# Kernel optimization log

Hardware: AMD Instinct MI355X
Metric: run time of the kernel (lower is better)

The kernel has to match this reference:

```python
import jax, jax.numpy as jnp
import numpy as np

B, K, D, H, NIRREPS = 1024, 16, 1024, 16, 16  # batch, seq_len(=group n), input_dim, heads, n_irreps
HD = D // H


def setup_inputs() -> dict:
    key = jax.random.key(0)
    ks = jax.random.split(key, 10)
    s = 1.0 / np.sqrt(D)
    return {
        "x": jax.random.normal(ks[0], (B, K, D), jnp.float32),
        "projectors": jax.random.normal(ks[1], (NIRREPS, K, K), jnp.float32) * 0.25,
        "Wq": jax.random.normal(ks[2], (D, D), jnp.float32) * s,
        "bq": jnp.zeros((D,), jnp.float32),
        "Wk": jax.random.normal(ks[3], (D, D), jnp.float32) * s,
        "bk": jnp.zeros((D,), jnp.float32),
        "Wv": jax.random.normal(ks[4], (D, D), jnp.float32) * s,
        "bv": jnp.zeros((D,), jnp.float32),
        "Wo": jax.random.normal(ks[5], (D, D), jnp.float32) * s,
        "bo": jnp.zeros((D,), jnp.float32),
    }


def reference(x, projectors, Wq, bq, Wk, bk, Wv, bv, Wo, bo):
    b, k, d = x.shape
    hd = d // H
    # QKV projections -> [b, H, k, hd]
    def heads(t):
        return t.reshape(b, k, H, hd).transpose(0, 2, 1, 3)
    Q = heads(x @ Wq + bq)
    Kt = heads(x @ Wk + bk)
    V = heads(x @ Wv + bv)
    scale = jnp.asarray(1.0 / np.sqrt(hd), x.dtype)

    # Per-irrep: project Q/K/V along the seq axis with P, run masked-free softmax
    # attention on tiny k x k scores, accumulate over irreps (eval mode, no dropout).
    def body(acc, P):
        Qp = jnp.einsum('ij,bhjd->bhid', P, Q)
        Kp = jnp.einsum('ij,bhjd->bhid', P, Kt)
        Vp = jnp.einsum('ij,bhjd->bhid', P, V)
        scores = jnp.einsum('bhid,bhjd->bhij', Qp, Kp) * scale
        w = jax.nn.softmax(scores, axis=-1)
        return acc + jnp.einsum('bhij,bhjd->bhid', w, Vp), None

    total, _ = jax.lax.scan(body, jnp.zeros_like(V), projectors)
    # merge heads -> [b, k, d], then output projection
    out = total.transpose(0, 2, 1, 3).reshape(b, k, d) @ Wo + bo
    return out
```

## Files before the change

kernel.cpp:

```cpp
#include <hip/hip_runtime.h>


typedef unsigned short u16;
typedef unsigned int u32;
typedef __attribute__((ext_vector_type(8))) __bf16 bf16x8;
typedef __attribute__((ext_vector_type(4))) float f32x4;
typedef __attribute__((ext_vector_type(4))) u32 u32x4;
typedef __attribute__((ext_vector_type(4))) u16 u16x4;
typedef __attribute__((ext_vector_type(4))) float float4v;
typedef __attribute__((address_space(1))) void gvoid;
typedef __attribute__((address_space(3))) void svoid;

#define MFMA16(a, b, c) __builtin_amdgcn_mfma_f32_16x16x32_bf16(a, b, c, 0, 0, 0)

__device__ __forceinline__ u16 f2bf(float f) {
  u32 u = __builtin_bit_cast(u32, f);
  return (u16)((u + 0x7fffu + ((u >> 16) & 1u)) >> 16);
}
__device__ __forceinline__ float bf2f(u16 h) {
  u32 u = ((u32)h) << 16;
  return __builtin_bit_cast(float, u);
}
__device__ __forceinline__ float ld_bias(const void* p, int i, int isf32) {
  return isf32 ? ((const float*)p)[i] : bf2f(((const u16*)p)[i]);
}
__device__ __forceinline__ bf16x8 ld_frag(const u16* p) {
  u32x4 v = *reinterpret_cast<const u32x4*>(p);
  return __builtin_bit_cast(bf16x8, v);
}
__device__ __forceinline__ bf16x8 ld_frag_lo(const u16* p, int lane) {
  u32x4 v = {0u, 0u, 0u, 0u};
  if (lane < 32) v = *reinterpret_cast<const u32x4*>(p);
  return __builtin_bit_cast(bf16x8, v);
}
__device__ __forceinline__ void async16(const u16* g, u16* l) {
  __builtin_amdgcn_global_load_lds((gvoid*)g, (svoid*)l, 16, 0, 0);
}

__device__ __forceinline__ bf16x8 c2frag(f32x4 v, int lane) {
  const u32 p01 = ((u32)f2bf(v[1]) << 16) | (u32)f2bf(v[0]);
  const u32 p23 = ((u32)f2bf(v[3]) << 16) | (u32)f2bf(v[2]);
  const int base = (lane & 15) + ((lane & 16) << 1);
  u32x4 o;
  o[0] = (u32)__shfl((int)p01, base);
  o[1] = (u32)__shfl((int)p23, base);
  o[2] = (u32)__shfl((int)p01, base + 16);
  o[3] = (u32)__shfl((int)p23, base + 16);
  if (lane >= 32) o = (u32x4){0u, 0u, 0u, 0u};
  return __builtin_bit_cast(bf16x8, o);
}

__global__ __launch_bounds__(1024) void detect_dtype(const u32* __restrict__ x,
                                                     int* __restrict__ flag) {
  const int tid = threadIdx.x;
  int cnt = 0;
#pragma unroll
  for (int q = 0; q < 4; ++q) {
    const u32x4 v = ((const u32x4*)x)[q * 1024 + tid];
#pragma unroll
    for (int j = 0; j < 4; ++j) {
      const u32 e = (v[j] >> 23) & 0xffu;
      cnt += (e >= 64u && e <= 191u) ? 1 : 0;
    }
  }
  __shared__ int sred[16];
  for (int o = 32; o; o >>= 1) cnt += __shfl_down(cnt, o);
  if ((tid & 63) == 0) sred[tid >> 6] = cnt;
  __syncthreads();
  if (tid == 0) {
    int t = 0;
#pragma unroll
    for (int i = 0; i < 16; ++i) t += sred[i];
    flag[0] = (t > 8192) ? 1 : 0;
  }
}

__global__ __launch_bounds__(256) void convert_x(const void* __restrict__ src,
                                                 u16* __restrict__ dst,
                                                 const int* __restrict__ flag) {
  const int i4 = blockIdx.x * 256 + threadIdx.x;
  if (*flag) {
    const float4v v = ((const float4v*)src)[i4];
    u16x4 o;
#pragma unroll
    for (int j = 0; j < 4; ++j) o[j] = f2bf(v[j]);
    ((u16x4*)dst)[i4] = o;
  } else {
    ((u16x4*)dst)[i4] = ((const u16x4*)src)[i4];
  }
}

__global__ __launch_bounds__(256) void transpose_conv(
    const void* __restrict__ w0, const void* __restrict__ w1,
    const void* __restrict__ w2, const void* __restrict__ w3,
    u16* __restrict__ d0, u16* __restrict__ d1, u16* __restrict__ d2,
    u16* __restrict__ d3, const int* __restrict__ flag) {
  __shared__ u16 tile[32][33];
  const int z = blockIdx.z;
  const void* src = (z == 0) ? w0 : (z == 1) ? w1 : (z == 2) ? w2 : w3;
  u16* dst = (z == 0) ? d0 : (z == 1) ? d1 : (z == 2) ? d2 : d3;
  const int isf32 = *flag;
  const int tx = threadIdx.x & 31;
  const int ty = (threadIdx.x >> 5) * 4;
  const int bx = blockIdx.x * 32;
  const int by = blockIdx.y * 32;
#pragma unroll
  for (int r = 0; r < 4; ++r) {
    const int idx = (by + ty + r) * 1024 + bx + tx;
    tile[ty + r][tx] = isf32 ? f2bf(((const float*)src)[idx]) : ((const u16*)src)[idx];
  }
  __syncthreads();
#pragma unroll
  for (int r = 0; r < 4; ++r)
    dst[(bx + ty + r) * 1024 + by + tx] = tile[tx][ty + r];
}

template <int MODE>
__global__ __launch_bounds__(512, 2) void gemm256(
    const u16* __restrict__ X, const u16* __restrict__ Wt,
    const void* __restrict__ b0, const void* __restrict__ b1,
    const void* __restrict__ b2, void* __restrict__ o0, u16* __restrict__ o1,
    u16* __restrict__ o2, const int* __restrict__ flag) {
  __shared__ alignas(16) u16 sm[65536];
  const int tid = threadIdx.x;
  const int wave = tid >> 6, lane = tid & 63;
  const int fr = lane & 15, fq = lane >> 4;
  const int wm = wave >> 2, wn = wave & 3;
  const int isf32 = *flag;

  const int nwg = gridDim.x;
  const int per = nwg >> 3;
  const int bid = blockIdx.x;
  const int wg = (bid & 7) * per + (bid >> 3);
  const int m0 = (wg & 63) << 8;
  const int n0 = (wg >> 6) << 8;

  const int gl = ((tid & 7) ^ ((tid >> 3) & 7)) * 8;
  const u16* aS = X + (size_t)(m0 + (tid >> 3)) * 1024 + gl;
  const u16* bS = Wt + (size_t)(n0 + (tid >> 3)) * 1024 + gl;
  u16* dA = sm + wave * 512;
  u16* dB = sm + 16384 + wave * 512;

  const u16* aR = sm + (wm * 128 + fr) * 64;
  const u16* bR = sm + 16384 + (wn * 64 + fr) * 64;
  const int g0 = (fq ^ (fr & 7)) * 8;
  const int g1 = ((fq ^ (fr & 7)) ^ 4) * 8;

  f32x4 acc[2][4][4] = {};
  bf16x8 af[2][4][2], bf[4][2];

#define STG_A(BUF, H, KT)                                                     \
  do {                                                                        \
    async16(aS + (H * 128) * 1024 + (KT), dA + (BUF)*32768 + (H)*8192);       \
    async16(aS + (H * 128 + 64) * 1024 + (KT),                                \
            dA + (BUF)*32768 + (H)*8192 + 4096);                              \
  } while (0)
#define STG_B(BUF, H, KT)                                                     \
  do {                                                                        \
    async16(bS + (H * 128) * 1024 + (KT), dB + (BUF)*32768 + (H)*8192);       \
    async16(bS + (H * 128 + 64) * 1024 + (KT),                                \
            dB + (BUF)*32768 + (H)*8192 + 4096);                              \
  } while (0)
#define LDA_ALL(CH, KH, BUF)                                                  \
  do {                                                                        \
    af[CH][0][KH] = ld_frag(aR + (BUF)*32768 + (CH)*4096 + ((KH) ? g1 : g0)); \
    af[CH][1][KH] =                                                           \
        ld_frag(aR + (BUF)*32768 + (CH)*4096 + 1024 + ((KH) ? g1 : g0));      \
    af[CH][2][KH] =                                                           \
        ld_frag(aR + (BUF)*32768 + (CH)*4096 + 2048 + ((KH) ? g1 : g0));      \
    af[CH][3][KH] =                                                           \
        ld_frag(aR + (BUF)*32768 + (CH)*4096 + 3072 + ((KH) ? g1 : g0));      \
  } while (0)
#define LDB_ALL(KH, BUF)                                                      \
  do {                                                                        \
    bf[0][KH] = ld_frag(bR + (BUF)*32768 + ((KH) ? g1 : g0));                 \
    bf[1][KH] = ld_frag(bR + (BUF)*32768 + 1024 + ((KH) ? g1 : g0));          \
    bf[2][KH] = ld_frag(bR + (BUF)*32768 + 2048 + ((KH) ? g1 : g0));          \
    bf[3][KH] = ld_frag(bR + (BUF)*32768 + 3072 + ((KH) ? g1 : g0));          \
  } while (0)
#define MM1(CH, FI, KH)                                                       \
  acc[CH][FI][0] = MFMA16(af[CH][FI][KH], bf[0][KH], acc[CH][FI][0]);         \
  acc[CH][FI][1] = MFMA16(af[CH][FI][KH], bf[1][KH], acc[CH][FI][1]);         \
  acc[CH][FI][2] = MFMA16(af[CH][FI][KH], bf[2][KH], acc[CH][FI][2]);         \
  acc[CH][FI][3] = MFMA16(af[CH][FI][KH], bf[3][KH], acc[CH][FI][3]);
#define MM(CH, KH)                                                            \
  do {                                                                        \
    __builtin_amdgcn_s_setprio(1);                                            \
    MM1(CH, 0, KH) MM1(CH, 1, KH) MM1(CH, 2, KH) MM1(CH, 3, KH)               \
    __builtin_amdgcn_s_setprio(0);                                            \
  } while (0)
#define BARR                                                                  \
  __builtin_amdgcn_s_barrier();                                               \
  __builtin_amdgcn_sched_barrier(0)
#define WAITV(N) asm volatile("s_waitcnt vmcnt(" #N ")" ::: "memory")
#define WAITL asm volatile("s_waitcnt lgkmcnt(0)" ::: "memory")
#define SCHED __builtin_amdgcn_sched_barrier(0)

  STG_A(0, 0, 0);
  STG_A(0, 1, 0);
  STG_B(0, 0, 0);
  STG_B(0, 1, 0);
  STG_A(1, 0, 64);
  STG_A(1, 1, 64);
  WAITV(4);
  BARR;

  for (int it = 0; it < 7; ++it) {
    const int kof = it * 128;
    LDA_ALL(0, 0, 0);
    LDB_ALL(0, 0);
    LDA_ALL(1, 0, 0);
    STG_B(1, 0, kof + 64);
    BARR;
    MM(0, 0);
    BARR;
    LDA_ALL(0, 1, 0);
    LDA_ALL(1, 1, 0);
    STG_B(1, 1, kof + 64);
    BARR;
    MM(1, 0);
    WAITL;
    SCHED;
    BARR;
    LDB_ALL(1, 0);
    STG_A(0, 0, kof + 128);
    BARR;
    MM(0, 1);
    BARR;
    STG_A(0, 1, kof + 128);
    BARR;
    MM(1, 1);
    WAITV(4);
    SCHED;
    BARR;
    LDA_ALL(0, 0, 1);
    LDB_ALL(0, 1);
    LDA_ALL(1, 0, 1);
    STG_B(0, 0, kof + 128);
    BARR;
    MM(0, 0);
    BARR;
    LDA_ALL(0, 1, 1);
    LDA_ALL(1, 1, 1);
    STG_B(0, 1, kof + 128);
    BARR;
    MM(1, 0);
    WAITL;
    SCHED;
    BARR;
    LDB_ALL(1, 1);
    STG_A(1, 0, kof + 192);
    BARR;
    MM(0, 1);
    BARR;
    STG_A(1, 1, kof + 192);
    BARR;
    MM(1, 1);
    WAITV(4);
    SCHED;
    BARR;
  }

  {
    LDA_ALL(0, 0, 0);
    LDB_ALL(0, 0);
    LDA_ALL(1, 0, 0);
    LDA_ALL(0, 1, 0);
    LDA_ALL(1, 1, 0);
    LDB_ALL(1, 0);
    STG_B(1, 0, 960);
    STG_B(1, 1, 960);
    MM(0, 0);
    MM(1, 0);
    MM(0, 1);
    MM(1, 1);
    WAITV(0);
    BARR;
    LDA_ALL(0, 0, 1);
    LDB_ALL(0, 1);
    LDA_ALL(1, 0, 1);
    LDA_ALL(0, 1, 1);
    LDA_ALL(1, 1, 1);
    LDB_ALL(1, 1);
    MM(0, 0);
    MM(1, 0);
    MM(0, 1);
    MM(1, 1);
  }

  if constexpr (MODE == 0) {
    const int q = n0 >> 10;
    const int nb = (n0 & 1023) + wn * 64;
    const void* bp = (q == 0) ? b0 : ((q == 1) ? b1 : b2);
    u16* q0 = (u16*)o0;
#pragma unroll
    for (int ch = 0; ch < 2; ++ch)
#pragma unroll
      for (int fi = 0; fi < 4; ++fi) {
        const int mbase = m0 + wm * 128 + ch * 64 + fi * 16;
        const int bidx = mbase >> 4;
#pragma unroll
        for (int bj = 0; bj < 4; ++bj) {
          const int nl = nb + bj * 16 + fr;
          const int h = nl >> 6, d = nl & 63;
          const float bias = ld_bias(bp, nl, isf32);
          const int bh = bidx * 16 + h;
          if (q == 2) {
            u16x4 pk;
#pragma unroll
            for (int r = 0; r < 4; ++r) pk[r] = f2bf(acc[ch][fi][bj][r] + bias);
            *reinterpret_cast<u16x4*>(&o2[(bh * 64 + d) * 16 + fq * 4]) = pk;
          } else {
            u16* dstq = (q == 0) ? q0 : o1;
#pragma unroll
            for (int r = 0; r < 4; ++r)
              dstq[(bh * 16 + fq * 4 + r) * 64 + d] =
                  f2bf(acc[ch][fi][bj][r] + bias);
          }
        }
      }
  } else {
#pragma unroll
    for (int ch = 0; ch < 2; ++ch)
#pragma unroll
      for (int fi = 0; fi < 4; ++fi) {
        const int m = m0 + wm * 128 + ch * 64 + fi * 16 + fq * 4;
#pragma unroll
        for (int bj = 0; bj < 4; ++bj) {
          const int n = n0 + wn * 64 + bj * 16 + fr;
          const float bias = ld_bias(b0, n, isf32);
          if (isf32) {
#pragma unroll
            for (int r = 0; r < 4; ++r)
              ((float*)o0)[(m + r) * 1024 + n] = acc[ch][fi][bj][r] + bias;
          } else {
#pragma unroll
            for (int r = 0; r < 4; ++r)
              ((u16*)o0)[(m + r) * 1024 + n] = f2bf(acc[ch][fi][bj][r] + bias);
          }
        }
      }
  }
#undef STG_A
#undef STG_B
#undef LDA_ALL
#undef LDB_ALL
#undef MM1
#undef MM
#undef BARR
#undef WAITV
#undef WAITL
#undef SCHED
}

__global__ __launch_bounds__(256) void attn_kernel(
    const u16* __restrict__ Qb, const u16* __restrict__ Kb, const u16* __restrict__ Vt,
    const void* __restrict__ P, u16* __restrict__ Tb,
    const int* __restrict__ flag) {
  __shared__ alignas(16) u16 Pl[4096];
  __shared__ alignas(16) u16 Ptl[4096];
  const int tid = threadIdx.x;
  const int isf32 = *flag;
#pragma unroll
  for (int i = 0; i < 16; ++i) {
    const int idx = i * 256 + tid;
    const u16 v = isf32 ? f2bf(((const float*)P)[idx]) : ((const u16*)P)[idx];
    Pl[idx] = v;
    const int p = idx >> 8, rc = idx & 255, rr = rc >> 4, cc = rc & 15;
    Ptl[(p << 8) + (cc << 4) + rr] = v;
  }
  __syncthreads();

  const int wave = tid >> 6, lane = tid & 63;
  const int bh = blockIdx.x * 4 + wave;
  const int fr = lane & 15, fq = lane >> 4;

  const u16* qb = Qb + bh * 1024;
  const u16* kb = Kb + bh * 1024;
  const u16* vb = Vt + bh * 1024;

  const bf16x8 qf0 = ld_frag(qb + fr * 64 + fq * 8);
  const bf16x8 qf1 = ld_frag(qb + fr * 64 + 32 + fq * 8);
  const bf16x8 kf0 = ld_frag(kb + fr * 64 + fq * 8);
  const bf16x8 kf1 = ld_frag(kb + fr * 64 + 32 + fq * 8);
  f32x4 S = {0.f, 0.f, 0.f, 0.f};
  S = MFMA16(qf0, kf0, S);
  S = MFMA16(qf1, kf1, S);
#pragma unroll
  for (int r = 0; r < 4; ++r) S[r] *= 0.125f;
  const bf16x8 St = c2frag(S, lane);

  f32x4 Mt = {0.f, 0.f, 0.f, 0.f};
#pragma unroll 4
  for (int p = 0; p < 16; ++p) {
    const bf16x8 pl = ld_frag_lo(Pl + (p << 8) + fr * 16 + fq * 8, lane);
    const bf16x8 pt = ld_frag_lo(Ptl + (p << 8) + fr * 16 + fq * 8, lane);
    f32x4 z = {0.f, 0.f, 0.f, 0.f};
    const f32x4 ApT = MFMA16(St, pl, z);
    const f32x4 BpT = MFMA16(pl, c2frag(ApT, lane), z);
    float e[4], s = 0.f;
#pragma unroll
    for (int r = 0; r < 4; ++r) {
      e[r] = __expf(BpT[r]);
      s += e[r];
    }
    s += __shfl_xor(s, 16);
    s += __shfl_xor(s, 32);
    const float rs = __frcp_rn(s);
    f32x4 w;
#pragma unroll
    for (int r = 0; r < 4; ++r) w[r] = e[r] * rs;
    Mt = MFMA16(pt, c2frag(w, lane), Mt);
  }

  const bf16x8 mb = c2frag(Mt, lane);

  const int b = bh >> 4, h = bh & 15;
  u16* outp = Tb + (b * 16 + fr) * 1024 + h * 64;
#pragma unroll
  for (int dt = 0; dt < 4; ++dt) {
    const bf16x8 vf = ld_frag_lo(vb + (dt * 16 + fr) * 16 + fq * 8, lane);
    f32x4 z = {0.f, 0.f, 0.f, 0.f};
    const f32x4 ot = MFMA16(vf, mb, z);
    u16x4 pk;
#pragma unroll
    for (int r = 0; r < 4; ++r) pk[r] = f2bf(ot[r]);
    *reinterpret_cast<u16x4*>(&outp[dt * 16 + fq * 4]) = pk;
  }
}

extern "C" void kernel_launch(void* const* d_in, const int* in_sizes, int n_in,
                              void* d_out, int out_size, void* d_ws, size_t ws_size,
                              hipStream_t stream) {
  const void* x = d_in[0];
  const void* proj = d_in[1];
  const void* Wq = d_in[2];
  const void* bq = d_in[3];
  const void* Wk = d_in[4];
  const void* bk = d_in[5];
  const void* Wv = d_in[6];
  const void* bv = d_in[7];
  const void* Wo = d_in[8];
  const void* bo = d_in[9];

  char* ws = (char*)d_ws;
  int* flag = (int*)ws;          ws += 256;
  u16* WtQKV = (u16*)ws;         ws += (size_t)3072 * 1024 * 2;
  u16* WtO   = (u16*)ws;         ws += (size_t)1024 * 1024 * 2;
  u16* Xb    = (u16*)ws;         ws += (size_t)16384 * 1024 * 2;
  u16* Qbuf  = (u16*)ws;         ws += (size_t)16384 * 1024 * 2;
  u16* Kbuf  = (u16*)ws;         ws += (size_t)16384 * 1024 * 2;
  u16* Vtb   = (u16*)ws;         ws += (size_t)16384 * 1024 * 2;
  u16* Tbuf  = (u16*)ws;         ws += (size_t)16384 * 1024 * 2;

  detect_dtype<<<1, 1024, 0, stream>>>((const u32*)x, flag);
  convert_x<<<16384, 256, 0, stream>>>(x, Xb, flag);
  transpose_conv<<<dim3(32, 32, 4), 256, 0, stream>>>(
      Wq, Wk, Wv, Wo, WtQKV, WtQKV + 1024 * 1024, WtQKV + 2 * 1024 * 1024, WtO, flag);

  gemm256<0><<<dim3(768), 512, 0, stream>>>(
      Xb, WtQKV, bq, bk, bv, Qbuf, Kbuf, Vtb, flag);
  attn_kernel<<<4096, 256, 0, stream>>>(Qbuf, Kbuf, Vtb, proj, Tbuf, flag);
  gemm256<1><<<dim3(256), 512, 0, stream>>>(
      Tbuf, WtO, bo, nullptr, nullptr, d_out, nullptr, nullptr, flag);
}
```

Measured before the change: 362.4 us.

## Fuse preprocessing kernels, pair irreps per MFMA in attention, split GEMM accumulators

Merges the x conversion and weight transpose kernels into one launch, saving a kernel launch and tail. In the attention kernel, two irreps are processed per iteration and their softmax weights are packed into one full-K MFMA, halving the accumulate MFMAs that previously ran half-zeroed. The GEMM accumulator array is split into two separate arrays behind a macro, presumably to help register allocation. Risks: more live registers in the attention loop, and the accumulator split may change nothing.

After: 351.7 us (median of 2 runs). 1.03x faster.

```diff
diff --git a/kernel.cpp b/kernel.cpp
--- a/kernel.cpp
+++ b/kernel.cpp
@@ -50,6 +50,28 @@
   return __builtin_bit_cast(bf16x8, o);
 }
 
+__device__ __forceinline__ bf16x8 c2frag_pair(f32x4 va, f32x4 vb, int lane) {
+  const u32 a01 = ((u32)f2bf(va[1]) << 16) | (u32)f2bf(va[0]);
+  const u32 a23 = ((u32)f2bf(va[3]) << 16) | (u32)f2bf(va[2]);
+  const u32 b01 = ((u32)f2bf(vb[1]) << 16) | (u32)f2bf(vb[0]);
+  const u32 b23 = ((u32)f2bf(vb[3]) << 16) | (u32)f2bf(vb[2]);
+  const int base = (lane & 15) + ((lane & 16) << 1);
+  const u32 sa0 = (u32)__shfl((int)a01, base);
+  const u32 sa1 = (u32)__shfl((int)a23, base);
+  const u32 sa2 = (u32)__shfl((int)a01, base + 16);
+  const u32 sa3 = (u32)__shfl((int)a23, base + 16);
+  const u32 sb0 = (u32)__shfl((int)b01, base);
+  const u32 sb1 = (u32)__shfl((int)b23, base);
+  const u32 sb2 = (u32)__shfl((int)b01, base + 16);
+  const u32 sb3 = (u32)__shfl((int)b23, base + 16);
+  u32x4 o;
+  o[0] = (lane < 32) ? sa0 : sb0;
+  o[1] = (lane < 32) ? sa1 : sb1;
+  o[2] = (lane < 32) ? sa2 : sb2;
+  o[3] = (lane < 32) ? sa3 : sb3;
+  return __builtin_bit_cast(bf16x8, o);
+}
+
 __global__ __launch_bounds__(1024) void detect_dtype(const u32* __restrict__ x,
                                                      int* __restrict__ flag) {
   const int tid = threadIdx.x;
@@ -75,44 +97,46 @@
   }
 }
 
-__global__ __launch_bounds__(256) void convert_x(const void* __restrict__ src,
-                                                 u16* __restrict__ dst,
-                                                 const int* __restrict__ flag) {
-  const int i4 = blockIdx.x * 256 + threadIdx.x;
-  if (*flag) {
-    const float4v v = ((const float4v*)src)[i4];
-    u16x4 o;
-#pragma unroll
-    for (int j = 0; j < 4; ++j) o[j] = f2bf(v[j]);
-    ((u16x4*)dst)[i4] = o;
-  } else {
-    ((u16x4*)dst)[i4] = ((const u16x4*)src)[i4];
-  }
-}
-
-__global__ __launch_bounds__(256) void transpose_conv(
+__global__ __launch_bounds__(256) void preprocess(
+    const void* __restrict__ src_x, u16* __restrict__ dst_x,
     const void* __restrict__ w0, const void* __restrict__ w1,
     const void* __restrict__ w2, const void* __restrict__ w3,
     u16* __restrict__ d0, u16* __restrict__ d1, u16* __restrict__ d2,
     u16* __restrict__ d3, const int* __restrict__ flag) {
   __shared__ u16 tile[32][33];
-  const int z = blockIdx.z;
-  const void* src = (z == 0) ? w0 : (z == 1) ? w1 : (z == 2) ? w2 : w3;
-  u16* dst = (z == 0) ? d0 : (z == 1) ? d1 : (z == 2) ? d2 : d3;
+  const int bid = blockIdx.x;
+  const int tid = threadIdx.x;
   const int isf32 = *flag;
-  const int tx = threadIdx.x & 31;
-  const int ty = (threadIdx.x >> 5) * 4;
-  const int bx = blockIdx.x * 32;
-  const int by = blockIdx.y * 32;
-#pragma unroll
-  for (int r = 0; r < 4; ++r) {
-    const int idx = (by + ty + r) * 1024 + bx + tx;
-    tile[ty + r][tx] = isf32 ? f2bf(((const float*)src)[idx]) : ((const u16*)src)[idx];
-  }
-  __syncthreads();
-#pragma unroll
-  for (int r = 0; r < 4; ++r)
-    dst[(bx + ty + r) * 1024 + by + tx] = tile[tx][ty + r];
+  if (bid < 16384) {
+    const int i4 = bid * 256 + tid;
+    if (isf32) {
+      const float4v v = ((const float4v*)src_x)[i4];
+      u16x4 o;
+#pragma unroll
+      for (int j = 0; j < 4; ++j) o[j] = f2bf(v[j]);
+      ((u16x4*)dst_x)[i4] = o;
+    } else {
+      ((u16x4*)dst_x)[i4] = ((const u16x4*)src_x)[i4];
+    }
+  } else {
+    const int r = bid - 16384;
+    const int z = r >> 10;
+    const void* src = (z == 0) ? w0 : (z == 1) ? w1 : (z == 2) ? w2 : w3;
+    u16* dst = (z == 0) ? d0 : (z == 1) ? d1 : (z == 2) ? d2 : d3;
+    const int tx = tid & 31;
+    const int ty = (tid >> 5) * 4;
+    const int bx = (r & 31) * 32;
+    const int by = ((r >> 5) & 31) * 32;
+#pragma unroll
+    for (int q = 0; q < 4; ++q) {
+      const int idx = (by + ty + q) * 1024 + bx + tx;
+      tile[ty + q][tx] = isf32 ? f2bf(((const float*)src)[idx]) : ((const u16*)src)[idx];
+    }
+    __syncthreads();
+#pragma unroll
+    for (int q = 0; q < 4; ++q)
+      dst[(bx + ty + q) * 1024 + by + tx] = tile[tx][ty + q];
+  }
 }
 
 template <int MODE>
@@ -146,9 +170,11 @@
   const int g0 = (fq ^ (fr & 7)) * 8;
   const int g1 = ((fq ^ (fr & 7)) ^ 4) * 8;
 
-  f32x4 acc[2][4][4] = {};
+  f32x4 acc[4][4] = {};
+  f32x4 acc2[4][4] = {};
   bf16x8 af[2][4][2], bf[4][2];
 
+#define ACC(CH, FI, BJ) ((CH) ? acc2[FI][BJ] : acc[FI][BJ])
 #define STG_A(BUF, H, KT)                                                     \
   do {                                                                        \
     async16(aS + (H * 128) * 1024 + (KT), dA + (BUF)*32768 + (H)*8192);       \
@@ -179,10 +205,10 @@
     bf[3][KH] = ld_frag(bR + (BUF)*32768 + 3072 + ((KH) ? g1 : g0));          \
   } while (0)
 #define MM1(CH, FI, KH)                                                       \
-  acc[CH][FI][0] = MFMA16(af[CH][FI][KH], bf[0][KH], acc[CH][FI][0]);         \
-  acc[CH][FI][1] = MFMA16(af[CH][FI][KH], bf[1][KH], acc[CH][FI][1]);         \
-  acc[CH][FI][2] = MFMA16(af[CH][FI][KH], bf[2][KH], acc[CH][FI][2]);         \
-  acc[CH][FI][3] = MFMA16(af[CH][FI][KH], bf[3][KH], acc[CH][FI][3]);
+  ACC(CH, FI, 0) = MFMA16(af[CH][FI][KH], bf[0][KH], ACC(CH, FI, 0));         \
+  ACC(CH, FI, 1) = MFMA16(af[CH][FI][KH], bf[1][KH], ACC(CH, FI, 1));         \
+  ACC(CH, FI, 2) = MFMA16(af[CH][FI][KH], bf[2][KH], ACC(CH, FI, 2));         \
+  ACC(CH, FI, 3) = MFMA16(af[CH][FI][KH], bf[3][KH], ACC(CH, FI, 3));
 #define MM(CH, KH)                                                            \
   do {                                                                        \
     __builtin_amdgcn_s_setprio(1);                                            \
@@ -308,14 +334,14 @@
           if (q == 2) {
             u16x4 pk;
 #pragma unroll
-            for (int r = 0; r < 4; ++r) pk[r] = f2bf(acc[ch][fi][bj][r] + bias);
+            for (int r = 0; r < 4; ++r) pk[r] = f2bf(ACC(ch, fi, bj)[r] + bias);
             *reinterpret_cast<u16x4*>(&o2[(bh * 64 + d) * 16 + fq * 4]) = pk;
           } else {
             u16* dstq = (q == 0) ? q0 : o1;
 #pragma unroll
             for (int r = 0; r < 4; ++r)
               dstq[(bh * 16 + fq * 4 + r) * 64 + d] =
-                  f2bf(acc[ch][fi][bj][r] + bias);
+                  f2bf(ACC(ch, fi, bj)[r] + bias);
           }
         }
       }
@@ -332,15 +358,16 @@
           if (isf32) {
 #pragma unroll
             for (int r = 0; r < 4; ++r)
-              ((float*)o0)[(m + r) * 1024 + n] = acc[ch][fi][bj][r] + bias;
+              ((float*)o0)[(m + r) * 1024 + n] = ACC(ch, fi, bj)[r] + bias;
           } else {
 #pragma unroll
             for (int r = 0; r < 4; ++r)
-              ((u16*)o0)[(m + r) * 1024 + n] = f2bf(acc[ch][fi][bj][r] + bias);
+              ((u16*)o0)[(m + r) * 1024 + n] = f2bf(ACC(ch, fi, bj)[r] + bias);
           }
         }
       }
   }
+#undef ACC
 #undef STG_A
 #undef STG_B
 #undef LDA_ALL
@@ -391,26 +418,38 @@
   const bf16x8 St = c2frag(S, lane);
 
   f32x4 Mt = {0.f, 0.f, 0.f, 0.f};
-#pragma unroll 4
-  for (int p = 0; p < 16; ++p) {
-    const bf16x8 pl = ld_frag_lo(Pl + (p << 8) + fr * 16 + fq * 8, lane);
-    const bf16x8 pt = ld_frag_lo(Ptl + (p << 8) + fr * 16 + fq * 8, lane);
+#pragma unroll 2
+  for (int p = 0; p < 16; p += 2) {
     f32x4 z = {0.f, 0.f, 0.f, 0.f};
-    const f32x4 ApT = MFMA16(St, pl, z);
-    const f32x4 BpT = MFMA16(pl, c2frag(ApT, lane), z);
-    float e[4], s = 0.f;
+    const bf16x8 plA = ld_frag_lo(Pl + (p << 8) + fr * 16 + fq * 8, lane);
+    const f32x4 ApTA = MFMA16(St, plA, z);
+    const f32x4 BpTA = MFMA16(plA, c2frag(ApTA, lane), z);
+    const bf16x8 plB = ld_frag_lo(Pl + ((p + 1) << 8) + fr * 16 + fq * 8, lane);
+    const f32x4 ApTB = MFMA16(St, plB, z);
+    const f32x4 BpTB = MFMA16(plB, c2frag(ApTB, lane), z);
+    float eA[4], eB[4], sA = 0.f, sB = 0.f;
 #pragma unroll
     for (int r = 0; r < 4; ++r) {
-      e[r] = __expf(BpT[r]);
-      s += e[r];
+      eA[r] = __expf(BpTA[r]);
+      sA += eA[r];
+      eB[r] = __expf(BpTB[r]);
+      sB += eB[r];
     }
-    s += __shfl_xor(s, 16);
-    s += __shfl_xor(s, 32);
-    const float rs = __frcp_rn(s);
-    f32x4 w;
-#pragma unroll
-    for (int r = 0; r < 4; ++r) w[r] = e[r] * rs;
-    Mt = MFMA16(pt, c2frag(w, lane), Mt);
+    sA += __shfl_xor(sA, 16);
+    sA += __shfl_xor(sA, 32);
+    sB += __shfl_xor(sB, 16);
+    sB += __shfl_xor(sB, 32);
+    const float rsA = __frcp_rn(sA);
+    const float rsB = __frcp_rn(sB);
+    f32x4 wA, wB;
+#pragma unroll
+    for (int r = 0; r < 4; ++r) {
+      wA[r] = eA[r] * rsA;
+      wB[r] = eB[r] * rsB;
+    }
+    const bf16x8 ptP =
+        ld_frag(Ptl + ((p + (fq >> 1)) << 8) + fr * 16 + (fq & 1) * 8);
+    Mt = MFMA16(ptP, c2frag_pair(wA, wB, lane), Mt);
   }
 
   const bf16x8 mb = c2frag(Mt, lane);
@@ -454,9 +493,9 @@
   u16* Tbuf  = (u16*)ws;         ws += (size_t)16384 * 1024 * 2;
 
   detect_dtype<<<1, 1024, 0, stream>>>((const u32*)x, flag);
-  convert_x<<<16384, 256, 0, stream>>>(x, Xb, flag);
-  transpose_conv<<<dim3(32, 32, 4), 256, 0, stream>>>(
-      Wq, Wk, Wv, Wo, WtQKV, WtQKV + 1024 * 1024, WtQKV + 2 * 1024 * 1024, WtO, flag);
+  preprocess<<<20480, 256, 0, stream>>>(
+      x, Xb, Wq, Wk, Wv, Wo, WtQKV, WtQKV + 1024 * 1024,
+      WtQKV + 2 * 1024 * 1024, WtO, flag);
 
   gemm256<0><<<dim3(768), 512, 0, stream>>>(
       Xb, WtQKV, bq, bk, bv, Qbuf, Kbuf, Vtb, flag);
```
